# Kernel tuning notes

Hardware: AMD Instinct MI355X
Metric: run time of the kernel (lower is better)

The kernel has to match this reference:

```python
import jax, jax.numpy as jnp
import numpy as np

N_QUBITS = 12
R = 1
EDGES = [(i, (i + 1) % N_QUBITS) for i in range(N_QUBITS)]
DIM = 2 ** N_QUBITS
BATCH = 64
_LET = 'abcdefghijklmnopqrstuvwxy'

_I4 = np.eye(4, dtype=np.float32)
_AD = np.fliplr(_I4).copy()                      # antidiagonal (XX imag pattern)
_YP = np.array([[0,0,0,1],[0,0,-1,0],[0,-1,0,0],[1,0,0,0]], dtype=np.float32)  # YY imag pattern
_CNOT = jnp.asarray(np.array([[1,0,0,0],[0,1,0,0],[0,0,0,1],[0,0,1,0]], dtype=np.complex64))
_k = np.arange(DIM)
# z_signs[i, k] = -1 if bit (n-i-1) of k is set, matching the torch buffer
_ZS = jnp.asarray(np.stack([1.0 - 2.0 * ((_k >> (N_QUBITS - i - 1)) & 1) for i in range(N_QUBITS)]).astype(np.float32))  # [n, 2^n]


def _c(r, i):
    return jax.lax.complex(r, i)


def rx_mat(t):
    c, s, z = jnp.cos(t / 2), jnp.sin(t / 2), jnp.zeros_like(t)
    real = jnp.stack([jnp.stack([c, z], -1), jnp.stack([z, c], -1)], -2)
    imag = jnp.stack([jnp.stack([z, -s], -1), jnp.stack([-s, z], -1)], -2)
    return _c(real, imag)


def ry_mat(t):
    c, s = jnp.cos(t / 2), jnp.sin(t / 2)
    real = jnp.stack([jnp.stack([c, -s], -1), jnp.stack([s, c], -1)], -2)
    return _c(real, jnp.zeros_like(real))


def rz_mat(t):
    p, z = t / 2, jnp.zeros_like(t)
    cp, sp = jnp.cos(p), jnp.sin(p)
    real = jnp.stack([jnp.stack([cp, z], -1), jnp.stack([z, cp], -1)], -2)
    imag = jnp.stack([jnp.stack([-sp, z], -1), jnp.stack([z, sp], -1)], -2)
    return _c(real, imag)


def ising_zz(t):
    p = t / 2
    c, s = jnp.cos(p), jnp.sin(p)
    dr = jnp.stack([c, c, c, c], -1)
    di = jnp.stack([-s, s, s, -s], -1)
    i4 = jnp.asarray(_I4)
    return _c(dr[..., :, None] * i4, di[..., :, None] * i4)


def ising_xx(t):
    c, s = jnp.cos(t / 2), jnp.sin(t / 2)
    return _c(c[..., None, None] * jnp.asarray(_I4), -s[..., None, None] * jnp.asarray(_AD))


def ising_yy(t):
    c, s = jnp.cos(t / 2), jnp.sin(t / 2)
    return _c(c[..., None, None] * jnp.asarray(_I4), s[..., None, None] * jnp.asarray(_YP))


def apply_1q(state, gate, q):
    # state [B, 2^n]; gate [2,2] or [B,2,2]; qubit axis sits at stride 2^q (matches torch view)
    B = state.shape[0]
    left, right = 2 ** (N_QUBITS - q - 1), 2 ** q
    s = state.reshape(B, left, 2, right)
    sub = 'bij' if gate.ndim == 3 else 'ij'
    return jnp.einsum(f'{sub},bljr->blir', gate, s).reshape(B, DIM)


def apply_2q(state, gate, q1, q2):
    # state [B, 2^n]; gate [4,4]; qubit index = tensor-axis index from MSB (matches torch permute path)
    if q1 > q2:
        q1, q2 = q2, q1
    B = state.shape[0]
    s = state.reshape((B,) + (2,) * N_QUBITS)
    g = gate.reshape(2, 2, 2, 2)
    ax = list(_LET[:N_QUBITS])
    out = ax.copy()
    u, v = ax[q1], ax[q2]
    out[q1], out[q2] = 'A', 'B'
    spec = f"AB{u}{v},Z{''.join(ax)}->Z{''.join(out)}"
    return jnp.einsum(spec, g, s).reshape(B, DIM)


def _forward(data, encoding_scale, encoding_bias, eta, ew_zz, ew_xx, ew_yy, nb_z, nb_x, nb_y, trainable_rots):
    B, n = data.shape
    # data-encoding gates, cached once per forward: angles [B, n] -> gates [B, n, 2, 2]
    rx_g = rx_mat(encoding_scale[:, 0] * data + encoding_bias[:, 0])
    ry_g = ry_mat(encoding_scale[:, 1] * data + encoding_bias[:, 1])
    rz_g = rz_mat(encoding_scale[:, 2] * data + encoding_bias[:, 2])
    state = jnp.zeros((B, DIM), jnp.complex64).at[:, 0].set(1.0)
    ising_fns = (ising_zz, ising_xx, ising_yy)
    ews = (ew_zz, ew_xx, ew_yy)
    nbs = (nb_z, nb_x, nb_y)
    bias_fns = (rz_mat, rx_mat, ry_mat)
    enc_types = ('full', 'xy', 'yz')
    for r in range(R):
        for b in range(3):  # blocks: ZZ, XX, YY
            bt = enc_types[b]
            # data encoding
            for q in range(n):
                if bt != 'yz':
                    state = apply_1q(state, rx_g[:, q], q)
                state = apply_1q(state, ry_g[:, q], q)
                if bt != 'xy':
                    state = apply_1q(state, rz_g[:, q], q)
            # Ising interaction on each edge
            theta = eta[r, b] * ews[b][r]            # [n_edges]
            egs = ising_fns[b](theta)                # [n_edges, 4, 4]
            for e, (i, j) in enumerate(EDGES):
                state = apply_2q(state, egs[e], i, j)
            # node biases (RZ / RX / RY matching the block)
            bgs = bias_fns[b](nbs[b][r])             # [n, 2, 2]
            for q in range(n):
                state = apply_1q(state, bgs[q], q)
            # trainable rotations rx, ry, rz per qubit
            rots = trainable_rots[r, b]              # [n, 3]
            rxg, ryg, rzg = rx_mat(rots[:, 0]), ry_mat(rots[:, 1]), rz_mat(rots[:, 2])
            for q in range(n):
                state = apply_1q(state, rxg[q], q)
                state = apply_1q(state, ryg[q], q)
                state = apply_1q(state, rzg[q], q)
            # CNOT entangling ring
            for q in range(n):
                state = apply_2q(state, _CNOT, q, (q + 1) % n)
    probs = state.real ** 2 + state.imag ** 2        # [B, 2^n]
    return probs @ _ZS.T                             # Pauli-Z expectations [B, n]


def setup_inputs() -> dict:
    key = jax.random.key(0)
    ks = jax.random.split(key, 12)
    n, E, f = N_QUBITS, len(EDGES), jnp.float32
    return {
        'data': jax.random.uniform(ks[0], (BATCH, n), f),
        'encoding_scale': jnp.pi * jnp.ones((n, 3), f) + 0.1 * jax.random.normal(ks[1], (n, 3), f),
        'encoding_bias': 0.1 * jax.random.normal(ks[2], (n, 3), f),
        'eta': 0.5 * jnp.ones((R, 3), f),
        'ew_zz': jnp.ones((R, E), f) + 0.1 * jax.random.normal(ks[3], (R, E), f),
        'ew_xx': jnp.ones((R, E), f) + 0.1 * jax.random.normal(ks[4], (R, E), f),
        'ew_yy': jnp.ones((R, E), f) + 0.1 * jax.random.normal(ks[5], (R, E), f),
        'nb_z': 0.1 * jax.random.normal(ks[6], (R, n), f),
        'nb_x': 0.1 * jax.random.normal(ks[7], (R, n), f),
        'nb_y': 0.1 * jax.random.normal(ks[8], (R, n), f),
        'trainable_rots': 0.1 * jax.random.normal(ks[9], (R, 3, n, 3), f),
    }


def reference(data, encoding_scale, encoding_bias, eta, ew_zz, ew_xx, ew_yy, nb_z, nb_x, nb_y, trainable_rots):
    return _forward(data, encoding_scale, encoding_bias, eta, ew_zz, ew_xx, ew_yy, nb_z, nb_x, nb_y, trainable_rots)
```

## Files before the change

kernel.cpp:

```cpp
#include <hip/hip_runtime.h>
#include <math.h>

#define NT 512
#define QDIM 4096

using F2 = float2;

__device__ __forceinline__ F2 cadd(F2 p, F2 q) { return make_float2(p.x + q.x, p.y + q.y); }
__device__ __forceinline__ F2 cmul(F2 p, F2 q) {
    return make_float2(p.x * q.x - p.y * q.y, p.x * q.y + p.y * q.x);
}

struct M2 { F2 a, b, c, d; };

__device__ __forceinline__ M2 mmul(M2 A, M2 B) {
    M2 R;
    R.a = cadd(cmul(A.a, B.a), cmul(A.b, B.c));
    R.b = cadd(cmul(A.a, B.b), cmul(A.b, B.d));
    R.c = cadd(cmul(A.c, B.a), cmul(A.d, B.c));
    R.d = cadd(cmul(A.c, B.b), cmul(A.d, B.d));
    return R;
}

__device__ __forceinline__ M2 mrx(float t) {
    float s, c; sincosf(0.5f * t, &s, &c);
    return { make_float2(c, 0), make_float2(0, -s), make_float2(0, -s), make_float2(c, 0) };
}
__device__ __forceinline__ M2 mry(float t) {
    float s, c; sincosf(0.5f * t, &s, &c);
    return { make_float2(c, 0), make_float2(-s, 0), make_float2(s, 0), make_float2(c, 0) };
}
__device__ __forceinline__ M2 mrz(float t) {
    float s, c; sincosf(0.5f * t, &s, &c);
    return { make_float2(c, -s), make_float2(0, 0), make_float2(0, 0), make_float2(c, s) };
}


template<int JB>
__device__ __forceinline__ void g1_reg(F2* amp, const F2* g) {
    const int m = 1 << JB;
    F2 m00 = g[0], m01 = g[1], m10 = g[2], m11 = g[3];
#pragma unroll
    for (int j = 0; j < 8; ++j)
        if (!(j & m)) {
            F2 a = amp[j], b = amp[j | m];
            amp[j]     = cadd(cmul(m00, a), cmul(m01, b));
            amp[j | m] = cadd(cmul(m10, a), cmul(m11, b));
        }
}

template<int LM>
__device__ __forceinline__ void g1_shfl(F2* amp, const F2* g, int lane) {
    bool u = (lane & LM) != 0;
    F2 gs = u ? g[3] : g[0];
    F2 gp = u ? g[2] : g[1];
#pragma unroll
    for (int j = 0; j < 8; ++j) {
        F2 p;
        p.x = __shfl_xor(amp[j].x, LM, 64);
        p.y = __shfl_xor(amp[j].y, LM, 64);
        amp[j] = cadd(cmul(gs, amp[j]), cmul(gp, p));
    }
}

__device__ __forceinline__ void swap_to_Lp(F2* amp, int tid, int l, int w, F2* b) {
#pragma unroll
    for (int j = 0; j < 8; ++j) b[j * 512 + tid] = amp[j];
    __syncthreads();
#pragma unroll
    for (int j = 0; j < 8; ++j) amp[j] = b[w * 512 + (j << 6) + l];
}

__device__ __forceinline__ void swap_to_L0(F2* amp, int tid, int l, int w, F2* b) {
#pragma unroll
    for (int j = 0; j < 8; ++j) b[w * 512 + (j << 6) + l] = amp[j];
    __syncthreads();
#pragma unroll
    for (int j = 0; j < 8; ++j) amp[j] = b[j * 512 + tid];
}

__device__ __forceinline__ F2 xyc(F2 a, F2 p, float c, float d) {
    return make_float2(fmaf(c, a.x, -d * p.y), fmaf(c, a.y, d * p.x));
}

template<int B1, int B0, bool YY>
__device__ __forceinline__ void xy_regj(F2* amp, F2 cs) {
    const int jm = (1 << B1) | (1 << B0);
    float c = cs.x, s = cs.y;
    F2 old[8];
#pragma unroll
    for (int j = 0; j < 8; ++j) old[j] = amp[j];
#pragma unroll
    for (int j = 0; j < 8; ++j) {
        int par = ((j >> B1) ^ (j >> B0)) & 1;
        float d = YY ? (par ? -s : s) : -s;
        amp[j] = xyc(old[j], old[j ^ jm], c, d);
    }
}

template<int LA, int LB, bool YY>
__device__ __forceinline__ void xy_shl(F2* amp, F2 cs, int lane) {
    const int LM = (1 << LA) | (1 << LB);
    int par = ((lane >> LA) ^ (lane >> LB)) & 1;
    float c = cs.x;
    float d = YY ? (par ? -cs.y : cs.y) : -cs.y;
#pragma unroll
    for (int j = 0; j < 8; ++j) {
        F2 p;
        p.x = __shfl_xor(amp[j].x, LM, 64);
        p.y = __shfl_xor(amp[j].y, LM, 64);
        amp[j] = xyc(amp[j], p, c, d);
    }
}

template<bool YY>
__device__ __forceinline__ void xy_cross98(F2* amp, F2 cs, int lane) {
    float c = cs.x, s = cs.y;
    int lp = (lane >> 5) & 1;
    F2 old[8];
#pragma unroll
    for (int j = 0; j < 8; ++j) old[j] = amp[j];
#pragma unroll
    for (int j = 0; j < 8; ++j) {
        F2 p;
        p.x = __shfl_xor(old[j ^ 1].x, 32, 64);
        p.y = __shfl_xor(old[j ^ 1].y, 32, 64);
        int par = (j & 1) ^ lp;
        float d = YY ? (par ? -s : s) : -s;
        amp[j] = xyc(old[j], p, c, d);
    }
}

template<bool YY>
__device__ __forceinline__ void xy_cross32(F2* amp, F2 cs, int lane) {
    float c = cs.x, s = cs.y;
    int lp = lane & 1;
    F2 old[8];
#pragma unroll
    for (int j = 0; j < 8; ++j) old[j] = amp[j];
#pragma unroll
    for (int j = 0; j < 8; ++j) {
        F2 p;
        p.x = __shfl_xor(old[j ^ 4].x, 1, 64);
        p.y = __shfl_xor(old[j ^ 4].y, 1, 64);
        int par = lp ^ ((j >> 2) & 1);
        float d = YY ? (par ? -s : s) : -s;
        amp[j] = xyc(old[j], p, c, d);
    }
}

template<bool YY>
__device__ __forceinline__ void xy_trip_11_0(F2* amp, F2 cs, int tid, F2* b) {
    float c = cs.x, s = cs.y;
    int wp = (tid >> 8) & 1;
#pragma unroll
    for (int j = 0; j < 8; ++j) b[j * 512 + tid] = amp[j];
    __syncthreads();
#pragma unroll
    for (int j = 0; j < 8; ++j) {
        F2 p = b[(j ^ 1) * 512 + (tid ^ 256)];
        int par = wp ^ (j & 1);
        float d = YY ? (par ? -s : s) : -s;
        amp[j] = xyc(amp[j], p, c, d);
    }
}

__device__ __forceinline__ void zz_all_Lp(F2* amp, const float* zhalf, int l, int w) {
    float zr[12];
#pragma unroll
    for (int e = 0; e < 12; ++e) zr[e] = zhalf[e];
#pragma unroll
    for (int j = 0; j < 8; ++j) {
        int k = (j << 9) | (l << 3) | w;
        float phi = 0.f;
#pragma unroll
        for (int e = 0; e < 12; ++e) {
            int hi = (e < 11) ? 11 - e : 11, lo = (e < 11) ? 10 - e : 0;
            phi += (((k >> hi) ^ (k >> lo)) & 1) ? zr[e] : -zr[e];
        }
        float sp, cp;
        __sincosf(phi, &sp, &cp);
        amp[j] = cmul(amp[j], make_float2(cp, sp));
    }
}

__device__ __forceinline__ int cnot_src(int k) {
#pragma unroll
    for (int e = 11; e >= 0; --e) {
        int hi = (e < 11) ? 11 - e : 11, lo = (e < 11) ? 10 - e : 0;
        if ((k >> hi) & 1) k ^= (1 << lo);
    }
    return k;
}

template<bool FROM_LP>
__device__ __forceinline__ void cnot_trip(F2* amp, int tid, int l, int w,
                                          const int* kslot, F2* b) {
#pragma unroll
    for (int j = 0; j < 8; ++j) {
        int slot = FROM_LP ? (w * 512 + (j << 6) + l) : (j * 512 + tid);
        b[slot] = amp[j];
    }
    __syncthreads();
#pragma unroll
    for (int j = 0; j < 8; ++j) amp[j] = b[kslot[j]];
}

__global__ __launch_bounds__(NT) void qsim_kernel(
    const float* __restrict__ data,
    const float* __restrict__ enc_scale,
    const float* __restrict__ enc_bias,
    const float* __restrict__ eta,
    const float* __restrict__ ew_zz,
    const float* __restrict__ ew_xx,
    const float* __restrict__ ew_yy,
    const float* __restrict__ nb_z,
    const float* __restrict__ nb_x,
    const float* __restrict__ nb_y,
    const float* __restrict__ trots,
    float* __restrict__ out)
{
    __shared__ F2 buf[2][QDIM];
    __shared__ F2 g1q[72][4];
    __shared__ F2 gis[24];
    __shared__ float zhalf[12];
    __shared__ float red[8][12];

    const int tid = threadIdx.x;
    const int l = tid & 63, w = tid >> 6;
    const int bat = blockIdx.x;

    if (tid < 36) {
        int b = tid / 12, q = tid % 12;
        float x  = data[bat * 12 + q];
        float ax = enc_scale[q * 3 + 0] * x + enc_bias[q * 3 + 0];
        float ay = enc_scale[q * 3 + 1] * x + enc_bias[q * 3 + 1];
        float az = enc_scale[q * 3 + 2] * x + enc_bias[q * 3 + 2];
        M2 M;
        if (b == 0)      M = mmul(mrz(az), mmul(mry(ay), mrx(ax)));
        else if (b == 1) M = mmul(mry(ay), mrx(ax));
        else             M = mmul(mrz(az), mry(ay));
        g1q[tid][0] = M.a; g1q[tid][1] = M.b; g1q[tid][2] = M.c; g1q[tid][3] = M.d;
    } else if (tid < 72) {
        int i = tid - 36, b = i / 12, q = i % 12;
        float nb = (b == 0) ? nb_z[q] : (b == 1) ? nb_x[q] : nb_y[q];
        M2 M0 = (b == 0) ? mrz(nb) : (b == 1) ? mrx(nb) : mry(nb);
        float t0 = trots[(b * 12 + q) * 3 + 0];
        float t1 = trots[(b * 12 + q) * 3 + 1];
        float t2 = trots[(b * 12 + q) * 3 + 2];
        M2 M = mmul(mrz(t2), mmul(mry(t1), mmul(mrx(t0), M0)));
        g1q[tid][0] = M.a; g1q[tid][1] = M.b; g1q[tid][2] = M.c; g1q[tid][3] = M.d;
    } else if (tid < 96) {
        int i = tid - 72, b = i / 12, e = i % 12;
        const float* ew = (b == 0) ? ew_xx : ew_yy;
        float th = eta[b + 1] * ew[e];
        float s, c; sincosf(0.5f * th, &s, &c);
        gis[i] = make_float2(c, s);
    } else if (tid < 108) {
        int e = tid - 96;
        zhalf[e] = 0.5f * eta[0] * ew_zz[e];
    }
    __syncthreads();

    F2 amp[8];
#pragma unroll
    for (int j = 0; j < 8; ++j) amp[j] = make_float2(0.f, 0.f);
    if (tid == 0) amp[0].x = 1.f;

    int kslot[8];
#pragma unroll
    for (int j = 0; j < 8; ++j) {
        int ks = cnot_src((tid << 3) | j);
        kslot[j] = (ks & 7) * 512 + (ks >> 3);
    }

    int sel = 0;
#define NB (&buf[(sel ^= 1) ^ 1][0])

    for (int blk = 0; blk < 3; ++blk) {
        const F2(*Ge)[4] = &g1q[blk * 12];
        const F2(*Gb)[4] = &g1q[36 + blk * 12];

        g1_reg<0>(amp, Ge[0]);  g1_reg<1>(amp, Ge[1]);  g1_reg<2>(amp, Ge[2]);
        g1_shfl<1>(amp, Ge[3], l);  g1_shfl<2>(amp, Ge[4], l);  g1_shfl<4>(amp, Ge[5], l);
        g1_shfl<8>(amp, Ge[6], l);  g1_shfl<16>(amp, Ge[7], l); g1_shfl<32>(amp, Ge[8], l);
        swap_to_Lp(amp, tid, l, w, NB);
        g1_reg<0>(amp, Ge[9]);  g1_reg<1>(amp, Ge[10]);  g1_reg<2>(amp, Ge[11]);

        if (blk == 0) {
            zz_all_Lp(amp, zhalf, l, w);
            g1_reg<0>(amp, Gb[9]);  g1_reg<1>(amp, Gb[10]);  g1_reg<2>(amp, Gb[11]);
            g1_shfl<1>(amp, Gb[3], l);  g1_shfl<2>(amp, Gb[4], l);  g1_shfl<4>(amp, Gb[5], l);
            g1_shfl<8>(amp, Gb[6], l);  g1_shfl<16>(amp, Gb[7], l); g1_shfl<32>(amp, Gb[8], l);
            swap_to_L0(amp, tid, l, w, NB);
            g1_reg<0>(amp, Gb[0]);  g1_reg<1>(amp, Gb[1]);  g1_reg<2>(amp, Gb[2]);
            cnot_trip<false>(amp, tid, l, w, kslot, NB);
        } else {
            const F2* G = (blk == 1) ? &gis[0] : &gis[12];
            if (blk == 1) {
                xy_regj<2,1,false>(amp, G[0]);
                xy_regj<1,0,false>(amp, G[1]);
                xy_cross98<false>(amp, G[2], l);
                xy_shl<5,4,false>(amp, G[3], l);
                xy_shl<4,3,false>(amp, G[4], l);
                xy_shl<3,2,false>(amp, G[5], l);
                xy_shl<2,1,false>(amp, G[6], l);
                xy_shl<1,0,false>(amp, G[7], l);
                swap_to_L0(amp, tid, l, w, NB);
                xy_cross32<false>(amp, G[8], l);
                xy_regj<2,1,false>(amp, G[9]);
                xy_regj<1,0,false>(amp, G[10]);
                xy_trip_11_0<false>(amp, G[11], tid, NB);
            } else {
                xy_regj<2,1,true>(amp, G[0]);
                xy_regj<1,0,true>(amp, G[1]);
                xy_cross98<true>(amp, G[2], l);
                xy_shl<5,4,true>(amp, G[3], l);
                xy_shl<4,3,true>(amp, G[4], l);
                xy_shl<3,2,true>(amp, G[5], l);
                xy_shl<2,1,true>(amp, G[6], l);
                xy_shl<1,0,true>(amp, G[7], l);
                swap_to_L0(amp, tid, l, w, NB);
                xy_cross32<true>(amp, G[8], l);
                xy_regj<2,1,true>(amp, G[9]);
                xy_regj<1,0,true>(amp, G[10]);
                xy_trip_11_0<true>(amp, G[11], tid, NB);
            }
            g1_reg<0>(amp, Gb[0]);  g1_reg<1>(amp, Gb[1]);  g1_reg<2>(amp, Gb[2]);
            g1_shfl<1>(amp, Gb[3], l);  g1_shfl<2>(amp, Gb[4], l);  g1_shfl<4>(amp, Gb[5], l);
            g1_shfl<8>(amp, Gb[6], l);  g1_shfl<16>(amp, Gb[7], l); g1_shfl<32>(amp, Gb[8], l);
            swap_to_Lp(amp, tid, l, w, NB);
            g1_reg<0>(amp, Gb[9]);  g1_reg<1>(amp, Gb[10]);  g1_reg<2>(amp, Gb[11]);
            cnot_trip<true>(amp, tid, l, w, kslot, NB);
        }
    }

    float acc[12];
#pragma unroll
    for (int i = 0; i < 12; ++i) acc[i] = 0.f;
#pragma unroll
    for (int j = 0; j < 8; ++j) {
        int k = (tid << 3) | j;
        float pr = amp[j].x * amp[j].x + amp[j].y * amp[j].y;
#pragma unroll
        for (int i = 0; i < 12; ++i)
            acc[i] += ((k >> (11 - i)) & 1) ? -pr : pr;
    }
#pragma unroll
    for (int off = 32; off > 0; off >>= 1)
#pragma unroll
        for (int i = 0; i < 12; ++i)
            acc[i] += __shfl_down(acc[i], off, 64);
    int wv = tid >> 6;
    if ((tid & 63) == 0)
#pragma unroll
        for (int i = 0; i < 12; ++i) red[wv][i] = acc[i];
    __syncthreads();
    if (tid < 12) {
        float s = 0.f;
#pragma unroll
        for (int ww = 0; ww < 8; ++ww) s += red[ww][tid];
        out[bat * 12 + tid] = s;
    }
}

extern "C" void kernel_launch(void* const* d_in, const int* in_sizes, int n_in,
                              void* d_out, int out_size, void* d_ws, size_t ws_size,
                              hipStream_t stream) {
    const float* data      = (const float*)d_in[0];
    const float* enc_scale = (const float*)d_in[1];
    const float* enc_bias  = (const float*)d_in[2];
    const float* eta       = (const float*)d_in[3];
    const float* ew_zz     = (const float*)d_in[4];
    const float* ew_xx     = (const float*)d_in[5];
    const float* ew_yy     = (const float*)d_in[6];
    const float* nb_z      = (const float*)d_in[7];
    const float* nb_x      = (const float*)d_in[8];
    const float* nb_y      = (const float*)d_in[9];
    const float* trots     = (const float*)d_in[10];
    float* out = (float*)d_out;

    int batch = out_size / 12;
    qsim_kernel<<<batch, NT, 0, stream>>>(data, enc_scale, enc_bias, eta,
                                          ew_zz, ew_xx, ew_yy,
                                          nb_z, nb_x, nb_y, trots, out);
}
```

Baseline: 109.6 us.

## Diagonalize XX/YY entanglers via basis change folded into single-qubit gates

Replaces the explicit XX and YY ising layers, which used many shuffles, register permutations and shared-memory exchanges, with the ZZ-style diagonal phase routine. The basis change (Hadamard for XX, a W matrix for YY) is folded into the neighbouring encoding and trainable single-qubit gate matrices. All three blocks then share one uniform code path: diagonal phase, 1q gates, swap, CNOT permutation. This removes shuffle and LDS traffic and one barrier per block, at the cost of evaluating the diagonal phases with sincos in every block, and it depends on the basis-change matrices being exactly correct.

```diff
diff --git a/kernel.cpp b/kernel.cpp
--- a/kernel.cpp
+++ b/kernel.cpp
@@ -35,6 +35,17 @@
     return { make_float2(c, -s), make_float2(0, 0), make_float2(0, 0), make_float2(c, s) };
 }
 
+#define RSQ2 0.70710678118654752f
+__device__ __forceinline__ M2 mH() {
+    return { make_float2(RSQ2, 0), make_float2(RSQ2, 0), make_float2(RSQ2, 0), make_float2(-RSQ2, 0) };
+}
+__device__ __forceinline__ M2 mW() {
+    return { make_float2(RSQ2, 0), make_float2(0, RSQ2), make_float2(RSQ2, 0), make_float2(0, -RSQ2) };
+}
+__device__ __forceinline__ M2 mWd() {
+    return { make_float2(RSQ2, 0), make_float2(RSQ2, 0), make_float2(0, -RSQ2), make_float2(0, RSQ2) };
+}
+
 
 template<int JB>
 __device__ __forceinline__ void g1_reg(F2* amp, const F2* g) {
@@ -79,93 +90,7 @@
     for (int j = 0; j < 8; ++j) amp[j] = b[j * 512 + tid];
 }
 
-__device__ __forceinline__ F2 xyc(F2 a, F2 p, float c, float d) {
-    return make_float2(fmaf(c, a.x, -d * p.y), fmaf(c, a.y, d * p.x));
-}
-
-template<int B1, int B0, bool YY>
-__device__ __forceinline__ void xy_regj(F2* amp, F2 cs) {
-    const int jm = (1 << B1) | (1 << B0);
-    float c = cs.x, s = cs.y;
-    F2 old[8];
-#pragma unroll
-    for (int j = 0; j < 8; ++j) old[j] = amp[j];
-#pragma unroll
-    for (int j = 0; j < 8; ++j) {
-        int par = ((j >> B1) ^ (j >> B0)) & 1;
-        float d = YY ? (par ? -s : s) : -s;
-        amp[j] = xyc(old[j], old[j ^ jm], c, d);
-    }
-}
-
-template<int LA, int LB, bool YY>
-__device__ __forceinline__ void xy_shl(F2* amp, F2 cs, int lane) {
-    const int LM = (1 << LA) | (1 << LB);
-    int par = ((lane >> LA) ^ (lane >> LB)) & 1;
-    float c = cs.x;
-    float d = YY ? (par ? -cs.y : cs.y) : -cs.y;
-#pragma unroll
-    for (int j = 0; j < 8; ++j) {
-        F2 p;
-        p.x = __shfl_xor(amp[j].x, LM, 64);
-        p.y = __shfl_xor(amp[j].y, LM, 64);
-        amp[j] = xyc(amp[j], p, c, d);
-    }
-}
-
-template<bool YY>
-__device__ __forceinline__ void xy_cross98(F2* amp, F2 cs, int lane) {
-    float c = cs.x, s = cs.y;
-    int lp = (lane >> 5) & 1;
-    F2 old[8];
-#pragma unroll
-    for (int j = 0; j < 8; ++j) old[j] = amp[j];
-#pragma unroll
-    for (int j = 0; j < 8; ++j) {
-        F2 p;
-        p.x = __shfl_xor(old[j ^ 1].x, 32, 64);
-        p.y = __shfl_xor(old[j ^ 1].y, 32, 64);
-        int par = (j & 1) ^ lp;
-        float d = YY ? (par ? -s : s) : -s;
-        amp[j] = xyc(old[j], p, c, d);
-    }
-}
-
-template<bool YY>
-__device__ __forceinline__ void xy_cross32(F2* amp, F2 cs, int lane) {
-    float c = cs.x, s = cs.y;
-    int lp = lane & 1;
-    F2 old[8];
-#pragma unroll
-    for (int j = 0; j < 8; ++j) old[j] = amp[j];
-#pragma unroll
-    for (int j = 0; j < 8; ++j) {
-        F2 p;
-        p.x = __shfl_xor(old[j ^ 4].x, 1, 64);
-        p.y = __shfl_xor(old[j ^ 4].y, 1, 64);
-        int par = lp ^ ((j >> 2) & 1);
-        float d = YY ? (par ? -s : s) : -s;
-        amp[j] = xyc(old[j], p, c, d);
-    }
-}
-
-template<bool YY>
-__device__ __forceinline__ void xy_trip_11_0(F2* amp, F2 cs, int tid, F2* b) {
-    float c = cs.x, s = cs.y;
-    int wp = (tid >> 8) & 1;
-#pragma unroll
-    for (int j = 0; j < 8; ++j) b[j * 512 + tid] = amp[j];
-    __syncthreads();
-#pragma unroll
-    for (int j = 0; j < 8; ++j) {
-        F2 p = b[(j ^ 1) * 512 + (tid ^ 256)];
-        int par = wp ^ (j & 1);
-        float d = YY ? (par ? -s : s) : -s;
-        amp[j] = xyc(amp[j], p, c, d);
-    }
-}
-
-__device__ __forceinline__ void zz_all_Lp(F2* amp, const float* zhalf, int l, int w) {
+__device__ __forceinline__ void diag_all_Lp(F2* amp, const float* zhalf, int l, int w) {
     float zr[12];
 #pragma unroll
     for (int e = 0; e < 12; ++e) zr[e] = zhalf[e];
@@ -193,14 +118,9 @@
     return k;
 }
 
-template<bool FROM_LP>
-__device__ __forceinline__ void cnot_trip(F2* amp, int tid, int l, int w,
-                                          const int* kslot, F2* b) {
-#pragma unroll
-    for (int j = 0; j < 8; ++j) {
-        int slot = FROM_LP ? (w * 512 + (j << 6) + l) : (j * 512 + tid);
-        b[slot] = amp[j];
-    }
+__device__ __forceinline__ void cnot_trip(F2* amp, int tid, const int* kslot, F2* b) {
+#pragma unroll
+    for (int j = 0; j < 8; ++j) b[j * 512 + tid] = amp[j];
     __syncthreads();
 #pragma unroll
     for (int j = 0; j < 8; ++j) amp[j] = b[kslot[j]];
@@ -222,8 +142,7 @@
 {
     __shared__ F2 buf[2][QDIM];
     __shared__ F2 g1q[72][4];
-    __shared__ F2 gis[24];
-    __shared__ float zhalf[12];
+    __shared__ float zhalf[3][12];
     __shared__ float red[8][12];
 
     const int tid = threadIdx.x;
@@ -238,8 +157,8 @@
         float az = enc_scale[q * 3 + 2] * x + enc_bias[q * 3 + 2];
         M2 M;
         if (b == 0)      M = mmul(mrz(az), mmul(mry(ay), mrx(ax)));
-        else if (b == 1) M = mmul(mry(ay), mrx(ax));
-        else             M = mmul(mrz(az), mry(ay));
+        else if (b == 1) M = mmul(mH(), mmul(mry(ay), mrx(ax)));
+        else             M = mmul(mW(), mmul(mrz(az), mry(ay)));
         g1q[tid][0] = M.a; g1q[tid][1] = M.b; g1q[tid][2] = M.c; g1q[tid][3] = M.d;
     } else if (tid < 72) {
         int i = tid - 36, b = i / 12, q = i % 12;
@@ -249,16 +168,13 @@
         float t1 = trots[(b * 12 + q) * 3 + 1];
         float t2 = trots[(b * 12 + q) * 3 + 2];
         M2 M = mmul(mrz(t2), mmul(mry(t1), mmul(mrx(t0), M0)));
+        if (b == 1)      M = mmul(M, mH());
+        else if (b == 2) M = mmul(M, mWd());
         g1q[tid][0] = M.a; g1q[tid][1] = M.b; g1q[tid][2] = M.c; g1q[tid][3] = M.d;
-    } else if (tid < 96) {
+    } else if (tid < 108) {
         int i = tid - 72, b = i / 12, e = i % 12;
-        const float* ew = (b == 0) ? ew_xx : ew_yy;
-        float th = eta[b + 1] * ew[e];
-        float s, c; sincosf(0.5f * th, &s, &c);
-        gis[i] = make_float2(c, s);
-    } else if (tid < 108) {
-        int e = tid - 96;
-        zhalf[e] = 0.5f * eta[0] * ew_zz[e];
+        const float* ew = (b == 0) ? ew_zz : (b == 1) ? ew_xx : ew_yy;
+        zhalf[b][e] = 0.5f * eta[b] * ew[e];
     }
     __syncthreads();
 
@@ -287,52 +203,15 @@
         swap_to_Lp(amp, tid, l, w, NB);
         g1_reg<0>(amp, Ge[9]);  g1_reg<1>(amp, Ge[10]);  g1_reg<2>(amp, Ge[11]);
 
-        if (blk == 0) {
-            zz_all_Lp(amp, zhalf, l, w);
-            g1_reg<0>(amp, Gb[9]);  g1_reg<1>(amp, Gb[10]);  g1_reg<2>(amp, Gb[11]);
-            g1_shfl<1>(amp, Gb[3], l);  g1_shfl<2>(amp, Gb[4], l);  g1_shfl<4>(amp, Gb[5], l);
-            g1_shfl<8>(amp, Gb[6], l);  g1_shfl<16>(amp, Gb[7], l); g1_shfl<32>(amp, Gb[8], l);
-            swap_to_L0(amp, tid, l, w, NB);
-            g1_reg<0>(amp, Gb[0]);  g1_reg<1>(amp, Gb[1]);  g1_reg<2>(amp, Gb[2]);
-            cnot_trip<false>(amp, tid, l, w, kslot, NB);
-        } else {
-            const F2* G = (blk == 1) ? &gis[0] : &gis[12];
-            if (blk == 1) {
-                xy_regj<2,1,false>(amp, G[0]);
-                xy_regj<1,0,false>(amp, G[1]);
-                xy_cross98<false>(amp, G[2], l);
-                xy_shl<5,4,false>(amp, G[3], l);
-                xy_shl<4,3,false>(amp, G[4], l);
-                xy_shl<3,2,false>(amp, G[5], l);
-                xy_shl<2,1,false>(amp, G[6], l);
-                xy_shl<1,0,false>(amp, G[7], l);
-                swap_to_L0(amp, tid, l, w, NB);
-                xy_cross32<false>(amp, G[8], l);
-                xy_regj<2,1,false>(amp, G[9]);
-                xy_regj<1,0,false>(amp, G[10]);
-                xy_trip_11_0<false>(amp, G[11], tid, NB);
-            } else {
-                xy_regj<2,1,true>(amp, G[0]);
-                xy_regj<1,0,true>(amp, G[1]);
-                xy_cross98<true>(amp, G[2], l);
-                xy_shl<5,4,true>(amp, G[3], l);
-                xy_shl<4,3,true>(amp, G[4], l);
-                xy_shl<3,2,true>(amp, G[5], l);
-                xy_shl<2,1,true>(amp, G[6], l);
-                xy_shl<1,0,true>(amp, G[7], l);
-                swap_to_L0(amp, tid, l, w, NB);
-                xy_cross32<true>(amp, G[8], l);
-                xy_regj<2,1,true>(amp, G[9]);
-                xy_regj<1,0,true>(amp, G[10]);
-                xy_trip_11_0<true>(amp, G[11], tid, NB);
-            }
-            g1_reg<0>(amp, Gb[0]);  g1_reg<1>(amp, Gb[1]);  g1_reg<2>(amp, Gb[2]);
-            g1_shfl<1>(amp, Gb[3], l);  g1_shfl<2>(amp, Gb[4], l);  g1_shfl<4>(amp, Gb[5], l);
-            g1_shfl<8>(amp, Gb[6], l);  g1_shfl<16>(amp, Gb[7], l); g1_shfl<32>(amp, Gb[8], l);
-            swap_to_Lp(amp, tid, l, w, NB);
-            g1_reg<0>(amp, Gb[9]);  g1_reg<1>(amp, Gb[10]);  g1_reg<2>(amp, Gb[11]);
-            cnot_trip<true>(amp, tid, l, w, kslot, NB);
-        }
+        diag_all_Lp(amp, zhalf[blk], l, w);
+
+        g1_reg<0>(amp, Gb[9]);  g1_reg<1>(amp, Gb[10]);  g1_reg<2>(amp, Gb[11]);
+        g1_shfl<1>(amp, Gb[3], l);  g1_shfl<2>(amp, Gb[4], l);  g1_shfl<4>(amp, Gb[5], l);
+        g1_shfl<8>(amp, Gb[6], l);  g1_shfl<16>(amp, Gb[7], l); g1_shfl<32>(amp, Gb[8], l);
+        swap_to_L0(amp, tid, l, w, NB);
+        g1_reg<0>(amp, Gb[0]);  g1_reg<1>(amp, Gb[1]);  g1_reg<2>(amp, Gb[2]);
+
+        cnot_trip(amp, tid, kslot, NB);
     }
 
     float acc[12];
```

Result: faster. 106.2 us (-3.1%).
